# Kernel optimization log

Measured on AMD Instinct MI355X. Metric: run time of the kernel, lower is better.

Reference implementation:

```python
import jax, jax.numpy as jnp
import numpy as np

TEMP1 = 4.0  # local_temp1 default


def setup_inputs() -> dict:
    key = jax.random.key(0)
    k1, k2 = jax.random.split(key)
    query = jax.random.normal(k1, (256, 768, 96), dtype=jnp.float32)
    context = jax.random.normal(k2, (256, 768, 19, 19), dtype=jnp.float32)
    return {"query": query, "context": context}


def reference(query, context):
    # query: [B, ndf, Q]; context: [B, ndf, ih, iw]
    B, ndf, Q = query.shape
    ih, iw = context.shape[2], context.shape[3]
    S = ih * iw
    ctx = context.reshape(B, ndf, S)            # [B, ndf, S]
    # attn = contextT @ query -> [B, S, Q]
    attn = jnp.einsum('bds,bdq->bsq', ctx, query)
    # softmax over query dim
    attn = jax.nn.softmax(attn, axis=-1)
    # transpose to [B, Q, S], temperature scale, softmax over source dim
    attn = jnp.swapaxes(attn, 1, 2) * TEMP1
    attn = jax.nn.softmax(attn, axis=-1)        # [B, Q, S]
    # weightedContext = context @ attn^T -> [B, ndf, Q]
    weighted_context = jnp.einsum('bds,bqs->bdq', ctx, attn)
    attn_map = attn.reshape(B, Q, ih, iw)
    return weighted_context, attn_map
```

## Files before the change

### kernel.cpp

```cpp
#include <hip/hip_runtime.h>

#define NB 256
#define NDF 768
#define NQ 96
#define NS 361
#define LDT 40
#define LDP 392
#define WSROW 368
#define WS_BYTES ((size_t)NB * NQ * WSROW * 2)

typedef short bf16x8_t __attribute__((ext_vector_type(8)));
typedef float f32x4_t __attribute__((ext_vector_type(4)));
typedef float f32x4u_t __attribute__((ext_vector_type(4), aligned(4)));
typedef unsigned int u32x2_t __attribute__((ext_vector_type(2)));
typedef unsigned int u32x4_t __attribute__((ext_vector_type(4)));

__device__ __forceinline__ unsigned pack_hi(unsigned b_, unsigned a_) {
    return __builtin_amdgcn_perm(b_, a_, 0x07060302u);
}
__device__ __forceinline__ unsigned short f2bf(float x) {
    unsigned u = __float_as_uint(x);
    u += 0x7FFFu + ((u >> 16) & 1u);
    return (unsigned short)(u >> 16);
}
__device__ __forceinline__ float bf2f(unsigned short h) {
    return __uint_as_float(((unsigned)h) << 16);
}

template<bool WSP>
__global__ __launch_bounds__(384, 3) void k1_gemm1_softmaxq(
    const float* __restrict__ Qg, const float* __restrict__ Cg,
    unsigned short* __restrict__ Wsb, float* __restrict__ AoutF)
{
    __shared__ unsigned short sQhi[NQ * LDT];
    __shared__ unsigned short sQlo[NQ * LDT];
    __shared__ unsigned short sShi[192 * LDT];
    __shared__ unsigned short sSlo[192 * LDT];

    const int b = blockIdx.x >> 1;
    const int h = blockIdx.x & 1;
    const int tid = threadIdx.x;
    const int wv = tid >> 6;
    const int lane = tid & 63;
    const int ll = lane & 15;
    const int lg = lane >> 4;
    const int s0 = 192 * h;
    const int qq  = tid % NQ;
    const int kqQ = tid / NQ;
    const int ssb = tid % 192;
    const int kqC = tid / 192;
    const int sAbs = s0 + ssb;
    const bool okC = (sAbs < NS);

    const float* __restrict__ qg = Qg + (size_t)b * NDF * NQ;
    const float* __restrict__ cg = Cg + (size_t)b * NDF * NS;

    f32x4_t acc[6][2];
#pragma unroll
    for (int i = 0; i < 6; ++i)
#pragma unroll
        for (int j = 0; j < 2; ++j) acc[i][j] = (f32x4_t)0.0f;

    float RQa[8], RCa[16], RQb[8], RCb[16];

#define LOADQ(K0, R) { \
    const float* p = qg + ((K0) + 4 * kqQ) * NQ + qq; \
    R[0] = p[0]; R[1] = p[NQ]; R[2] = p[2 * NQ]; R[3] = p[3 * NQ]; \
    const float* p2 = p + 16 * NQ; \
    R[4] = p2[0]; R[5] = p2[NQ]; R[6] = p2[2 * NQ]; R[7] = p2[3 * NQ]; }

#define LOADC(K0, R) { \
    const float* p = cg + ((K0) + 4 * kqC) * NS + sAbs; \
    _Pragma("unroll") \
    for (int j = 0; j < 4; ++j) { \
        const float* pj = p + j * 8 * NS; \
        R[4*j+0] = okC ? pj[0] : 0.0f; \
        R[4*j+1] = okC ? pj[NS] : 0.0f; \
        R[4*j+2] = okC ? pj[2*NS] : 0.0f; \
        R[4*j+3] = okC ? pj[3*NS] : 0.0f; } }

#define STOREQC(RQ, RC) { \
    _Pragma("unroll") \
    for (int t = 0; t < 2; ++t) { \
        unsigned u0 = __float_as_uint(RQ[4*t+0]), u1 = __float_as_uint(RQ[4*t+1]); \
        unsigned u2 = __float_as_uint(RQ[4*t+2]), u3 = __float_as_uint(RQ[4*t+3]); \
        float l0 = RQ[4*t+0] - __uint_as_float(u0 & 0xFFFF0000u); \
        float l1 = RQ[4*t+1] - __uint_as_float(u1 & 0xFFFF0000u); \
        float l2 = RQ[4*t+2] - __uint_as_float(u2 & 0xFFFF0000u); \
        float l3 = RQ[4*t+3] - __uint_as_float(u3 & 0xFFFF0000u); \
        u32x2_t hi, lo; \
        hi[0] = pack_hi(u1, u0); hi[1] = pack_hi(u3, u2); \
        lo[0] = pack_hi(__float_as_uint(l1), __float_as_uint(l0)); \
        lo[1] = pack_hi(__float_as_uint(l3), __float_as_uint(l2)); \
        int off = qq * LDT + 4 * (kqQ + 4 * t); \
        *(u32x2_t*)&sQhi[off] = hi; \
        *(u32x2_t*)&sQlo[off] = lo; } \
    _Pragma("unroll") \
    for (int j = 0; j < 4; ++j) { \
        unsigned u0 = __float_as_uint(RC[4*j+0]), u1 = __float_as_uint(RC[4*j+1]); \
        unsigned u2 = __float_as_uint(RC[4*j+2]), u3 = __float_as_uint(RC[4*j+3]); \
        float l0 = RC[4*j+0] - __uint_as_float(u0 & 0xFFFF0000u); \
        float l1 = RC[4*j+1] - __uint_as_float(u1 & 0xFFFF0000u); \
        float l2 = RC[4*j+2] - __uint_as_float(u2 & 0xFFFF0000u); \
        float l3 = RC[4*j+3] - __uint_as_float(u3 & 0xFFFF0000u); \
        u32x2_t hi, lo; \
        hi[0] = pack_hi(u1, u0); hi[1] = pack_hi(u3, u2); \
        lo[0] = pack_hi(__float_as_uint(l1), __float_as_uint(l0)); \
        lo[1] = pack_hi(__float_as_uint(l3), __float_as_uint(l2)); \
        int off = ssb * LDT + 4 * (kqC + 2 * j); \
        *(u32x2_t*)&sShi[off] = hi; \
        *(u32x2_t*)&sSlo[off] = lo; } }

#define FRAGMFMA() { \
    bf16x8_t Bhi[2], Blo[2]; \
    _Pragma("unroll") \
    for (int nt = 0; nt < 2; ++nt) { \
        int row = 32 * wv + 16 * nt + ll; \
        Bhi[nt] = *(const bf16x8_t*)&sShi[row * LDT + 8 * lg]; \
        Blo[nt] = *(const bf16x8_t*)&sSlo[row * LDT + 8 * lg]; } \
    _Pragma("unroll") \
    for (int mt = 0; mt < 6; ++mt) { \
        int row = 16 * mt + ll; \
        bf16x8_t Ahi = *(const bf16x8_t*)&sQhi[row * LDT + 8 * lg]; \
        bf16x8_t Alo = *(const bf16x8_t*)&sQlo[row * LDT + 8 * lg]; \
        _Pragma("unroll") \
        for (int nt = 0; nt < 2; ++nt) { \
            acc[mt][nt] = __builtin_amdgcn_mfma_f32_16x16x32_bf16(Ahi, Bhi[nt], acc[mt][nt], 0, 0, 0); \
            acc[mt][nt] = __builtin_amdgcn_mfma_f32_16x16x32_bf16(Ahi, Blo[nt], acc[mt][nt], 0, 0, 0); \
            acc[mt][nt] = __builtin_amdgcn_mfma_f32_16x16x32_bf16(Alo, Bhi[nt], acc[mt][nt], 0, 0, 0); } } }

    LOADQ(0, RQa); LOADC(0, RCa);
    for (int k0 = 0; k0 < NDF; k0 += 64) {
        STOREQC(RQa, RCa);
        __syncthreads();
        if (k0 + 32 < NDF) { LOADQ(k0 + 32, RQb); LOADC(k0 + 32, RCb); }
        FRAGMFMA();
        __syncthreads();
        STOREQC(RQb, RCb);
        __syncthreads();
        if (k0 + 64 < NDF) { LOADQ(k0 + 64, RQa); LOADC(k0 + 64, RCa); }
        FRAGMFMA();
        __syncthreads();
    }
#undef LOADQ
#undef LOADC
#undef STOREQC
#undef FRAGMFMA

#pragma unroll
    for (int nt = 0; nt < 2; ++nt) {
        float m = -3.0e38f;
#pragma unroll
        for (int mt = 0; mt < 6; ++mt)
#pragma unroll
            for (int r = 0; r < 4; ++r) m = fmaxf(m, acc[mt][nt][r]);
        m = fmaxf(m, __shfl_xor(m, 16));
        m = fmaxf(m, __shfl_xor(m, 32));
        float sum = 0.0f;
#pragma unroll
        for (int mt = 0; mt < 6; ++mt)
#pragma unroll
            for (int r = 0; r < 4; ++r) {
                float e = __expf(acc[mt][nt][r] - m);
                acc[mt][nt][r] = e;
                sum += e;
            }
        sum += __shfl_xor(sum, 16);
        sum += __shfl_xor(sum, 32);
        float inv = 4.0f / sum;
#pragma unroll
        for (int mt = 0; mt < 6; ++mt)
#pragma unroll
            for (int r = 0; r < 4; ++r) acc[mt][nt][r] *= inv;
    }

    if constexpr (WSP) {
        unsigned short* wr = Wsb + (size_t)b * NQ * WSROW;
#pragma unroll
        for (int mt = 0; mt < 6; ++mt)
#pragma unroll
            for (int nt = 0; nt < 2; ++nt)
#pragma unroll
                for (int r = 0; r < 4; ++r) {
                    int q = 16 * mt + 4 * lg + r;
                    int s = s0 + 32 * wv + 16 * nt + ll;
                    if (s < NS) wr[q * WSROW + s] = f2bf(acc[mt][nt][r]);
                }
    } else {
        float* aout = AoutF + (size_t)b * NQ * NS;
#pragma unroll
        for (int mt = 0; mt < 6; ++mt)
#pragma unroll
            for (int nt = 0; nt < 2; ++nt)
#pragma unroll
                for (int r = 0; r < 4; ++r) {
                    int q = 16 * mt + 4 * lg + r;
                    int s = s0 + 32 * wv + 16 * nt + ll;
                    if (s < NS) aout[(size_t)q * NS + s] = acc[mt][nt][r];
                }
    }
}

__global__ __launch_bounds__(256) void k15_softmaxs(float* __restrict__ Aout)
{
    const int b = blockIdx.x;
    const int q = blockIdx.y * 4 + (threadIdx.x >> 6);
    const int lane = threadIdx.x & 63;
    float* __restrict__ row = Aout + ((size_t)b * NQ + q) * NS;
    const int c0 = 6 * lane;

    float v[6];
    if (c0 + 5 < NS) {
        f32x4u_t t = *(const f32x4u_t*)(row + c0);
        v[0] = t[0]; v[1] = t[1]; v[2] = t[2]; v[3] = t[3];
        v[4] = row[c0 + 4]; v[5] = row[c0 + 5];
    } else {
#pragma unroll
        for (int i = 0; i < 6; ++i) v[i] = (c0 + i < NS) ? row[c0 + i] : -INFINITY;
    }
    float m = v[0];
#pragma unroll
    for (int i = 1; i < 6; ++i) m = fmaxf(m, v[i]);
#pragma unroll
    for (int o = 1; o < 64; o <<= 1) m = fmaxf(m, __shfl_xor(m, o));
    float e[6], sum = 0.0f;
#pragma unroll
    for (int i = 0; i < 6; ++i) { e[i] = __expf(v[i] - m); sum += e[i]; }
#pragma unroll
    for (int o = 1; o < 64; o <<= 1) sum += __shfl_xor(sum, o);
    float inv = 1.0f / sum;
#pragma unroll
    for (int i = 0; i < 6; ++i) if (c0 + i < NS) row[c0 + i] = e[i] * inv;
}

template<bool FUSED>
__global__ __launch_bounds__(512, 4) void k2_gemm2(
    const float* __restrict__ Cg, const unsigned short* __restrict__ Wsb,
    const float* __restrict__ AttnF, float* __restrict__ Wout, float* __restrict__ AoutF)
{
    extern __shared__ char smem2[];
    unsigned short* sP = (unsigned short*)smem2;
    unsigned* sPd = (unsigned*)smem2;
    float* sMax = (float*)(smem2 + NQ * LDP * 2);
    float* sInv = sMax + NQ;

    const int b = blockIdx.x >> 2;
    const int quarter = blockIdx.x & 3;
    const int tid = threadIdx.x;
    const int wv = tid >> 6;
    const int lane = tid & 63;
    const int ll = lane & 15;
    const int lg = lane >> 4;

    if constexpr (FUSED) {
        const unsigned* __restrict__ wsd = (const unsigned*)(Wsb + (size_t)b * NQ * WSROW);
        for (int i = tid; i < NQ * 184; i += 512) {
            int r = i / 184, c = i - r * 184;
            sPd[r * 196 + c] = wsd[i];
        }
        for (int i = tid; i < NQ * 12; i += 512) {
            int r = i / 12, c = i - r * 12;
            sPd[r * 196 + 184 + c] = 0;
        }
        __syncthreads();

        const int l32 = tid & 31;
        const int rbase = tid >> 5;
#pragma unroll
        for (int pass = 0; pass < 6; ++pass) {
            int row = pass * 16 + rbase;
            float m = -3.0e38f;
#pragma unroll
            for (int j = 0; j < 6; ++j) {
                int dw = l32 + 32 * j;
                if (dw < 184) {
                    unsigned u = sPd[row * 196 + dw];
                    float v0 = bf2f((unsigned short)(u & 0xFFFFu));
                    float v1 = bf2f((unsigned short)(u >> 16));
                    if (2 * dw < NS) m = fmaxf(m, v0);
                    if (2 * dw + 1 < NS) m = fmaxf(m, v1);
                }
            }
#pragma unroll
            for (int o = 1; o < 32; o <<= 1) m = fmaxf(m, __shfl_xor(m, o));
            if (l32 == 0) sMax[row] = m;
        }
        __syncthreads();
#pragma unroll
        for (int pass = 0; pass < 6; ++pass) {
            int row = pass * 16 + rbase;
            float m = sMax[row];
            float sum = 0.0f;
#pragma unroll
            for (int j = 0; j < 6; ++j) {
                int dw = l32 + 32 * j;
                if (dw < 184) {
                    unsigned u = sPd[row * 196 + dw];
                    float v0 = bf2f((unsigned short)(u & 0xFFFFu));
                    float v1 = bf2f((unsigned short)(u >> 16));
                    float e0 = (2 * dw < NS) ? __expf(v0 - m) : 0.0f;
                    float e1 = (2 * dw + 1 < NS) ? __expf(v1 - m) : 0.0f;
                    sum += e0 + e1;
                    sPd[row * 196 + dw] = ((unsigned)f2bf(e1) << 16) | (unsigned)f2bf(e0);
                }
            }
#pragma unroll
            for (int o = 1; o < 32; o <<= 1) sum += __shfl_xor(sum, o);
            if (l32 == 0) sInv[row] = sum;
        }
        __syncthreads();
        if (tid < NQ) sInv[tid] = 1.0f / sInv[tid];
        __syncthreads();
        if (quarter == 0) {
            float* aout = AoutF + (size_t)b * NQ * NS;
            for (int i = tid; i < NQ * NS; i += 512) {
                int q = i / NS, s = i - q * NS;
                aout[i] = bf2f(sP[q * LDP + s]) * sInv[q];
            }
        }
    } else {
        const float* __restrict__ attn = AttnF + (size_t)b * NQ * NS;
        for (int i = tid; i < NQ * 181; i += 512) {
            int row = i / 181, p = i - row * 181;
            float x0 = attn[row * NS + 2 * p];
            float x1 = (p < 180) ? attn[row * NS + 2 * p + 1] : 0.0f;
            unsigned r0 = __float_as_uint(x0) + 0x8000u;
            unsigned r1 = __float_as_uint(x1) + 0x8000u;
            sPd[row * 196 + p] = pack_hi(r1, r0);
        }
        for (int i = tid; i < NQ * 15; i += 512) {
            int row = i / 15, p = i - row * 15;
            sPd[row * 196 + 181 + p] = 0;
        }
        __syncthreads();
    }

    f32x4_t acc[3][3];
#pragma unroll
    for (int i = 0; i < 3; ++i)
#pragma unroll
        for (int j = 0; j < 3; ++j) acc[i][j] = (f32x4_t)0.0f;

    const float* __restrict__ cq = Cg + (size_t)b * NDF * NS + (size_t)(quarter * 192) * NS;
    const int dw = wv >> 1, qw = wv & 1;

#pragma unroll
    for (int c = 0; c < 12; ++c) {
        bf16x8_t Bf[3];
#pragma unroll
        for (int nt = 0; nt < 3; ++nt) {
            int row = 16 * (3 * qw + nt) + ll;
            Bf[nt] = *(const bf16x8_t*)&sP[row * LDP + 32 * c + 8 * lg];
        }
#pragma unroll
        for (int i = 0; i < 3; ++i) {
            int d = 16 * (3 * dw + i) + ll;
            const float* ap = cq + (size_t)d * NS + 32 * c + 8 * lg;
            u32x4_t u;
            if (c < 11) {
                f32x4u_t a0 = *(const f32x4u_t*)ap;
                f32x4u_t a1 = *(const f32x4u_t*)(ap + 4);
                u[0] = pack_hi(__float_as_uint(a0[1]), __float_as_uint(a0[0]));
                u[1] = pack_hi(__float_as_uint(a0[3]), __float_as_uint(a0[2]));
                u[2] = pack_hi(__float_as_uint(a1[1]), __float_as_uint(a1[0]));
                u[3] = pack_hi(__float_as_uint(a1[3]), __float_as_uint(a1[2]));
            } else {
                float t[8];
#pragma unroll
                for (int e = 0; e < 8; ++e) {
                    int s = 352 + 8 * lg + e;
                    t[e] = (s < NS) ? ap[e] : 0.0f;
                }
                u[0] = pack_hi(__float_as_uint(t[1]), __float_as_uint(t[0]));
                u[1] = pack_hi(__float_as_uint(t[3]), __float_as_uint(t[2]));
                u[2] = pack_hi(__float_as_uint(t[5]), __float_as_uint(t[4]));
                u[3] = pack_hi(__float_as_uint(t[7]), __float_as_uint(t[6]));
            }
            bf16x8_t Af = __builtin_bit_cast(bf16x8_t, u);
#pragma unroll
            for (int nt = 0; nt < 3; ++nt)
                acc[i][nt] = __builtin_amdgcn_mfma_f32_16x16x32_bf16(Af, Bf[nt], acc[i][nt], 0, 0, 0);
        }
    }

    float* wout = Wout + (size_t)b * NDF * NQ;
    float invq[3];
#pragma unroll
    for (int nt = 0; nt < 3; ++nt) {
        if constexpr (FUSED) invq[nt] = sInv[16 * (3 * qw + nt) + ll];
        else invq[nt] = 1.0f;
    }
#pragma unroll
    for (int i = 0; i < 3; ++i)
#pragma unroll
        for (int nt = 0; nt < 3; ++nt)
#pragma unroll
            for (int r = 0; r < 4; ++r) {
                int d = quarter * 192 + 16 * (3 * dw + i) + 4 * lg + r;
                int q = 16 * (3 * qw + nt) + ll;
                wout[(size_t)d * NQ + q] = acc[i][nt][r] * invq[nt];
            }
}

extern "C" void kernel_launch(void* const* d_in, const int* in_sizes, int n_in,
                              void* d_out, int out_size, void* d_ws, size_t ws_size,
                              hipStream_t stream) {
    const float* Qg = (const float*)d_in[0];
    const float* Cg = (const float*)d_in[1];
    float* Wout = (float*)d_out;
    float* Aout = Wout + (size_t)NB * NDF * NQ;

    const int smem2 = NQ * LDP * 2 + NQ * 8;

    if (ws_size >= WS_BYTES) {
        unsigned short* wsb = (unsigned short*)d_ws;
        k1_gemm1_softmaxq<true><<<dim3(NB * 2), dim3(384), 0, stream>>>(Qg, Cg, wsb, nullptr);
        (void)hipFuncSetAttribute((const void*)k2_gemm2<true>,
                                  hipFuncAttributeMaxDynamicSharedMemorySize, smem2);
        k2_gemm2<true><<<dim3(NB * 4), dim3(512), smem2, stream>>>(Cg, wsb, nullptr, Wout, Aout);
    } else {
        k1_gemm1_softmaxq<false><<<dim3(NB * 2), dim3(384), 0, stream>>>(Qg, Cg, nullptr, Aout);
        k15_softmaxs<<<dim3(NB, 24), dim3(256), 0, stream>>>(Aout);
        (void)hipFuncSetAttribute((const void*)k2_gemm2<false>,
                                  hipFuncAttributeMaxDynamicSharedMemorySize, smem2);
        k2_gemm2<false><<<dim3(NB * 4), dim3(512), smem2, stream>>>(Cg, nullptr, Aout, Wout, Aout);
    }
}
```

Measured before the change: 229.4 us.

## Cache bf16 context in workspace from k1 so k2 reads half the bytes

Kernel 1, which already reads the fp32 context for the first GEMM, now also writes a truncated bf16 copy of it into a padded workspace buffer. Kernel 2 then loads bf16 fragments directly instead of re-reading and packing the fp32 context. This halves the context read traffic in k2 but adds a write of the same size in k1. The C-load mapping also changes so each thread handles two adjacent source columns, and the fallback paths change their rounding and load code slightly. This path only runs when the workspace is large enough to hold the copy.

```diff
diff --git a/kernel.cpp b/kernel.cpp
--- a/kernel.cpp
+++ b/kernel.cpp
@@ -7,7 +7,10 @@
 #define LDT 40
 #define LDP 392
 #define WSROW 368
-#define WS_BYTES ((size_t)NB * NQ * WSROW * 2)
+#define CSROW 368
+#define WS_LOG_BYTES ((size_t)NB * NQ * WSROW * 2)
+#define WS_CTX_BYTES ((size_t)NB * NDF * CSROW * 2)
+#define WS_FULL_BYTES (WS_LOG_BYTES + WS_CTX_BYTES)
 
 typedef short bf16x8_t __attribute__((ext_vector_type(8)));
 typedef float f32x4_t __attribute__((ext_vector_type(4)));
@@ -27,10 +30,11 @@
     return __uint_as_float(((unsigned)h) << 16);
 }
 
-template<bool WSP>
+template<int MODE>
 __global__ __launch_bounds__(384, 3) void k1_gemm1_softmaxq(
     const float* __restrict__ Qg, const float* __restrict__ Cg,
-    unsigned short* __restrict__ Wsb, float* __restrict__ AoutF)
+    unsigned short* __restrict__ WsLog, unsigned* __restrict__ WsCtxD,
+    float* __restrict__ AoutF)
 {
     __shared__ unsigned short sQhi[NQ * LDT];
     __shared__ unsigned short sQlo[NQ * LDT];
@@ -47,13 +51,17 @@
     const int s0 = 192 * h;
     const int qq  = tid % NQ;
     const int kqQ = tid / NQ;
-    const int ssb = tid % 192;
-    const int kqC = tid / 192;
-    const int sAbs = s0 + ssb;
-    const bool okC = (sAbs < NS);
+    const int sp  = tid % 96;
+    const int kqb = tid / 96;
+    const int sA0 = s0 + 2 * sp;
+    const bool ok0 = (sA0 < NS);
+    const bool ok1 = (sA0 + 1 < NS);
+    const int wsCol = 96 * h + sp;
+    const bool wok = (MODE == 2) && (wsCol < 184);
 
     const float* __restrict__ qg = Qg + (size_t)b * NDF * NQ;
     const float* __restrict__ cg = Cg + (size_t)b * NDF * NS;
+    unsigned* __restrict__ wscd = (MODE == 2) ? (WsCtxD + (size_t)b * NDF * 184) : nullptr;
 
     f32x4_t acc[6][2];
 #pragma unroll
@@ -61,7 +69,8 @@
 #pragma unroll
         for (int j = 0; j < 2; ++j) acc[i][j] = (f32x4_t)0.0f;
 
-    float RQa[8], RCa[16], RQb[8], RCb[16];
+    float RQa[8], RQb[8];
+    float RCa[16], RCb[16];
 
 #define LOADQ(K0, R) { \
     const float* p = qg + ((K0) + 4 * kqQ) * NQ + qq; \
@@ -70,46 +79,58 @@
     R[4] = p2[0]; R[5] = p2[NQ]; R[6] = p2[2 * NQ]; R[7] = p2[3 * NQ]; }
 
 #define LOADC(K0, R) { \
-    const float* p = cg + ((K0) + 4 * kqC) * NS + sAbs; \
     _Pragma("unroll") \
-    for (int j = 0; j < 4; ++j) { \
-        const float* pj = p + j * 8 * NS; \
-        R[4*j+0] = okC ? pj[0] : 0.0f; \
-        R[4*j+1] = okC ? pj[NS] : 0.0f; \
-        R[4*j+2] = okC ? pj[2*NS] : 0.0f; \
-        R[4*j+3] = okC ? pj[3*NS] : 0.0f; } }
-
-#define STOREQC(RQ, RC) { \
+    for (int k2 = 0; k2 < 2; ++k2) { \
+        const float* p = cg + ((K0) + 4 * (kqb + 4 * k2)) * NS; \
+        _Pragma("unroll") \
+        for (int j = 0; j < 4; ++j) { \
+            const float* pj = p + j * NS; \
+            R[(k2 * 4 + j) * 2 + 0] = ok0 ? pj[sA0] : 0.0f; \
+            R[(k2 * 4 + j) * 2 + 1] = ok1 ? pj[sA0 + 1] : 0.0f; } } }
+
+#define STOREQ(R) { \
     _Pragma("unroll") \
     for (int t = 0; t < 2; ++t) { \
-        unsigned u0 = __float_as_uint(RQ[4*t+0]), u1 = __float_as_uint(RQ[4*t+1]); \
-        unsigned u2 = __float_as_uint(RQ[4*t+2]), u3 = __float_as_uint(RQ[4*t+3]); \
-        float l0 = RQ[4*t+0] - __uint_as_float(u0 & 0xFFFF0000u); \
-        float l1 = RQ[4*t+1] - __uint_as_float(u1 & 0xFFFF0000u); \
-        float l2 = RQ[4*t+2] - __uint_as_float(u2 & 0xFFFF0000u); \
-        float l3 = RQ[4*t+3] - __uint_as_float(u3 & 0xFFFF0000u); \
+        unsigned u0 = __float_as_uint(R[4*t+0]), u1 = __float_as_uint(R[4*t+1]); \
+        unsigned u2 = __float_as_uint(R[4*t+2]), u3 = __float_as_uint(R[4*t+3]); \
+        float l0 = R[4*t+0] - __uint_as_float(u0 & 0xFFFF0000u); \
+        float l1 = R[4*t+1] - __uint_as_float(u1 & 0xFFFF0000u); \
+        float l2 = R[4*t+2] - __uint_as_float(u2 & 0xFFFF0000u); \
+        float l3 = R[4*t+3] - __uint_as_float(u3 & 0xFFFF0000u); \
         u32x2_t hi, lo; \
         hi[0] = pack_hi(u1, u0); hi[1] = pack_hi(u3, u2); \
         lo[0] = pack_hi(__float_as_uint(l1), __float_as_uint(l0)); \
         lo[1] = pack_hi(__float_as_uint(l3), __float_as_uint(l2)); \
         int off = qq * LDT + 4 * (kqQ + 4 * t); \
         *(u32x2_t*)&sQhi[off] = hi; \
-        *(u32x2_t*)&sQlo[off] = lo; } \
+        *(u32x2_t*)&sQlo[off] = lo; } }
+
+#define STOREC(K0, R) { \
     _Pragma("unroll") \
-    for (int j = 0; j < 4; ++j) { \
-        unsigned u0 = __float_as_uint(RC[4*j+0]), u1 = __float_as_uint(RC[4*j+1]); \
-        unsigned u2 = __float_as_uint(RC[4*j+2]), u3 = __float_as_uint(RC[4*j+3]); \
-        float l0 = RC[4*j+0] - __uint_as_float(u0 & 0xFFFF0000u); \
-        float l1 = RC[4*j+1] - __uint_as_float(u1 & 0xFFFF0000u); \
-        float l2 = RC[4*j+2] - __uint_as_float(u2 & 0xFFFF0000u); \
-        float l3 = RC[4*j+3] - __uint_as_float(u3 & 0xFFFF0000u); \
-        u32x2_t hi, lo; \
-        hi[0] = pack_hi(u1, u0); hi[1] = pack_hi(u3, u2); \
-        lo[0] = pack_hi(__float_as_uint(l1), __float_as_uint(l0)); \
-        lo[1] = pack_hi(__float_as_uint(l3), __float_as_uint(l2)); \
-        int off = ssb * LDT + 4 * (kqC + 2 * j); \
-        *(u32x2_t*)&sShi[off] = hi; \
-        *(u32x2_t*)&sSlo[off] = lo; } }
+    for (int k2 = 0; k2 < 2; ++k2) { \
+        const int kq = kqb + 4 * k2; \
+        unsigned u[4][2]; float l[4][2]; \
+        _Pragma("unroll") \
+        for (int j = 0; j < 4; ++j) { \
+            _Pragma("unroll") \
+            for (int s1 = 0; s1 < 2; ++s1) { \
+                float x = R[(k2 * 4 + j) * 2 + s1]; \
+                u[j][s1] = __float_as_uint(x); \
+                l[j][s1] = x - __uint_as_float(u[j][s1] & 0xFFFF0000u); } } \
+        _Pragma("unroll") \
+        for (int s1 = 0; s1 < 2; ++s1) { \
+            u32x2_t hi, lo; \
+            hi[0] = pack_hi(u[1][s1], u[0][s1]); \
+            hi[1] = pack_hi(u[3][s1], u[2][s1]); \
+            lo[0] = pack_hi(__float_as_uint(l[1][s1]), __float_as_uint(l[0][s1])); \
+            lo[1] = pack_hi(__float_as_uint(l[3][s1]), __float_as_uint(l[2][s1])); \
+            int off = (2 * sp + s1) * LDT + 4 * kq; \
+            *(u32x2_t*)&sShi[off] = hi; \
+            *(u32x2_t*)&sSlo[off] = lo; } \
+        if (wok) { \
+            _Pragma("unroll") \
+            for (int j = 0; j < 4; ++j) \
+                wscd[(size_t)((K0) + 4 * kq + j) * 184 + wsCol] = pack_hi(u[j][1], u[j][0]); } } }
 
 #define FRAGMFMA() { \
     bf16x8_t Bhi[2], Blo[2]; \
@@ -131,12 +152,12 @@
 
     LOADQ(0, RQa); LOADC(0, RCa);
     for (int k0 = 0; k0 < NDF; k0 += 64) {
-        STOREQC(RQa, RCa);
+        STOREQ(RQa); STOREC(k0, RCa);
         __syncthreads();
         if (k0 + 32 < NDF) { LOADQ(k0 + 32, RQb); LOADC(k0 + 32, RCb); }
         FRAGMFMA();
         __syncthreads();
-        STOREQC(RQb, RCb);
+        STOREQ(RQb); STOREC(k0 + 32, RCb);
         __syncthreads();
         if (k0 + 64 < NDF) { LOADQ(k0 + 64, RQa); LOADC(k0 + 64, RCa); }
         FRAGMFMA();
@@ -144,7 +165,8 @@
     }
 #undef LOADQ
 #undef LOADC
-#undef STOREQC
+#undef STOREQ
+#undef STOREC
 #undef FRAGMFMA
 
 #pragma unroll
@@ -174,8 +196,8 @@
             for (int r = 0; r < 4; ++r) acc[mt][nt][r] *= inv;
     }
 
-    if constexpr (WSP) {
-        unsigned short* wr = Wsb + (size_t)b * NQ * WSROW;
+    if constexpr (MODE >= 1) {
+        unsigned short* wr = WsLog + (size_t)b * NQ * WSROW;
 #pragma unroll
         for (int mt = 0; mt < 6; ++mt)
 #pragma unroll
@@ -210,14 +232,8 @@
     const int c0 = 6 * lane;
 
     float v[6];
-    if (c0 + 5 < NS) {
-        f32x4u_t t = *(const f32x4u_t*)(row + c0);
-        v[0] = t[0]; v[1] = t[1]; v[2] = t[2]; v[3] = t[3];
-        v[4] = row[c0 + 4]; v[5] = row[c0 + 5];
-    } else {
-#pragma unroll
-        for (int i = 0; i < 6; ++i) v[i] = (c0 + i < NS) ? row[c0 + i] : -INFINITY;
-    }
+#pragma unroll
+    for (int i = 0; i < 6; ++i) v[i] = (c0 + i < NS) ? row[c0 + i] : -INFINITY;
     float m = v[0];
 #pragma unroll
     for (int i = 1; i < 6; ++i) m = fmaxf(m, v[i]);
@@ -233,9 +249,10 @@
     for (int i = 0; i < 6; ++i) if (c0 + i < NS) row[c0 + i] = e[i] * inv;
 }
 
-template<bool FUSED>
+template<int MODE>
 __global__ __launch_bounds__(512, 4) void k2_gemm2(
-    const float* __restrict__ Cg, const unsigned short* __restrict__ Wsb,
+    const float* __restrict__ Cg, const unsigned short* __restrict__ WsLog,
+    const unsigned short* __restrict__ WsCtx,
     const float* __restrict__ AttnF, float* __restrict__ Wout, float* __restrict__ AoutF)
 {
     extern __shared__ char smem2[];
@@ -252,8 +269,8 @@
     const int ll = lane & 15;
     const int lg = lane >> 4;
 
-    if constexpr (FUSED) {
-        const unsigned* __restrict__ wsd = (const unsigned*)(Wsb + (size_t)b * NQ * WSROW);
+    if constexpr (MODE >= 1) {
+        const unsigned* __restrict__ wsd = (const unsigned*)(WsLog + (size_t)b * NQ * WSROW);
         for (int i = tid; i < NQ * 184; i += 512) {
             int r = i / 184, c = i - r * 184;
             sPd[r * 196 + c] = wsd[i];
@@ -324,9 +341,7 @@
             int row = i / 181, p = i - row * 181;
             float x0 = attn[row * NS + 2 * p];
             float x1 = (p < 180) ? attn[row * NS + 2 * p + 1] : 0.0f;
-            unsigned r0 = __float_as_uint(x0) + 0x8000u;
-            unsigned r1 = __float_as_uint(x1) + 0x8000u;
-            sPd[row * 196 + p] = pack_hi(r1, r0);
+            sPd[row * 196 + p] = pack_hi(__float_as_uint(x1), __float_as_uint(x0));
         }
         for (int i = tid; i < NQ * 15; i += 512) {
             int row = i / 15, p = i - row * 15;
@@ -341,8 +356,10 @@
 #pragma unroll
         for (int j = 0; j < 3; ++j) acc[i][j] = (f32x4_t)0.0f;
 
+    const int dw = wv >> 1, qw = wv & 1;
     const float* __restrict__ cq = Cg + (size_t)b * NDF * NS + (size_t)(quarter * 192) * NS;
-    const int dw = wv >> 1, qw = wv & 1;
+    const unsigned short* __restrict__ cb =
+        (MODE == 2) ? (WsCtx + ((size_t)b * NDF + quarter * 192) * CSROW) : nullptr;
 
 #pragma unroll
     for (int c = 0; c < 12; ++c) {
@@ -355,28 +372,37 @@
 #pragma unroll
         for (int i = 0; i < 3; ++i) {
             int d = 16 * (3 * dw + i) + ll;
-            const float* ap = cq + (size_t)d * NS + 32 * c + 8 * lg;
-            u32x4_t u;
-            if (c < 11) {
-                f32x4u_t a0 = *(const f32x4u_t*)ap;
-                f32x4u_t a1 = *(const f32x4u_t*)(ap + 4);
-                u[0] = pack_hi(__float_as_uint(a0[1]), __float_as_uint(a0[0]));
-                u[1] = pack_hi(__float_as_uint(a0[3]), __float_as_uint(a0[2]));
-                u[2] = pack_hi(__float_as_uint(a1[1]), __float_as_uint(a1[0]));
-                u[3] = pack_hi(__float_as_uint(a1[3]), __float_as_uint(a1[2]));
+            bf16x8_t Af;
+            if constexpr (MODE == 2) {
+                if (c < 11 || lg < 2) {
+                    Af = *(const bf16x8_t*)&cb[(size_t)d * CSROW + 32 * c + 8 * lg];
+                } else {
+                    Af = (bf16x8_t)0;
+                }
             } else {
-                float t[8];
-#pragma unroll
-                for (int e = 0; e < 8; ++e) {
-                    int s = 352 + 8 * lg + e;
-                    t[e] = (s < NS) ? ap[e] : 0.0f;
-                }
-                u[0] = pack_hi(__float_as_uint(t[1]), __float_as_uint(t[0]));
-                u[1] = pack_hi(__float_as_uint(t[3]), __float_as_uint(t[2]));
-                u[2] = pack_hi(__float_as_uint(t[5]), __float_as_uint(t[4]));
-                u[3] = pack_hi(__float_as_uint(t[7]), __float_as_uint(t[6]));
-            }
-            bf16x8_t Af = __builtin_bit_cast(bf16x8_t, u);
+                const float* ap = cq + (size_t)d * NS + 32 * c + 8 * lg;
+                u32x4_t u;
+                if (c < 11) {
+                    f32x4u_t a0 = *(const f32x4u_t*)ap;
+                    f32x4u_t a1 = *(const f32x4u_t*)(ap + 4);
+                    u[0] = pack_hi(__float_as_uint(a0[1]), __float_as_uint(a0[0]));
+                    u[1] = pack_hi(__float_as_uint(a0[3]), __float_as_uint(a0[2]));
+                    u[2] = pack_hi(__float_as_uint(a1[1]), __float_as_uint(a1[0]));
+                    u[3] = pack_hi(__float_as_uint(a1[3]), __float_as_uint(a1[2]));
+                } else {
+                    float t[8];
+#pragma unroll
+                    for (int e = 0; e < 8; ++e) {
+                        int s = 352 + 8 * lg + e;
+                        t[e] = (s < NS) ? ap[e] : 0.0f;
+                    }
+                    u[0] = pack_hi(__float_as_uint(t[1]), __float_as_uint(t[0]));
+                    u[1] = pack_hi(__float_as_uint(t[3]), __float_as_uint(t[2]));
+                    u[2] = pack_hi(__float_as_uint(t[5]), __float_as_uint(t[4]));
+                    u[3] = pack_hi(__float_as_uint(t[7]), __float_as_uint(t[6]));
+                }
+                Af = __builtin_bit_cast(bf16x8_t, u);
+            }
 #pragma unroll
             for (int nt = 0; nt < 3; ++nt)
                 acc[i][nt] = __builtin_amdgcn_mfma_f32_16x16x32_bf16(Af, Bf[nt], acc[i][nt], 0, 0, 0);
@@ -387,7 +413,7 @@
     float invq[3];
 #pragma unroll
     for (int nt = 0; nt < 3; ++nt) {
-        if constexpr (FUSED) invq[nt] = sInv[16 * (3 * qw + nt) + ll];
+        if constexpr (MODE >= 1) invq[nt] = sInv[16 * (3 * qw + nt) + ll];
         else invq[nt] = 1.0f;
     }
 #pragma unroll
@@ -412,17 +438,27 @@
 
     const int smem2 = NQ * LDP * 2 + NQ * 8;
 
-    if (ws_size >= WS_BYTES) {
-        unsigned short* wsb = (unsigned short*)d_ws;
-        k1_gemm1_softmaxq<true><<<dim3(NB * 2), dim3(384), 0, stream>>>(Qg, Cg, wsb, nullptr);
-        (void)hipFuncSetAttribute((const void*)k2_gemm2<true>,
+    if (ws_size >= WS_FULL_BYTES) {
+        unsigned short* wsLog = (unsigned short*)d_ws;
+        unsigned* wsCtxD = (unsigned*)((char*)d_ws + WS_LOG_BYTES);
+        k1_gemm1_softmaxq<2><<<dim3(NB * 2), dim3(384), 0, stream>>>(Qg, Cg, wsLog, wsCtxD, nullptr);
+        (void)hipFuncSetAttribute((const void*)k2_gemm2<2>,
                                   hipFuncAttributeMaxDynamicSharedMemorySize, smem2);
-        k2_gemm2<true><<<dim3(NB * 4), dim3(512), smem2, stream>>>(Cg, wsb, nullptr, Wout, Aout);
+        k2_gemm2<2><<<dim3(NB * 4), dim3(512), smem2, stream>>>(
+            Cg, wsLog, (const unsigned short*)wsCtxD, nullptr, Wout, Aout);
+    } else if (ws_size >= WS_LOG_BYTES) {
+        unsigned short* wsLog = (unsigned short*)d_ws;
+        k1_gemm1_softmaxq<1><<<dim3(NB * 2), dim3(384), 0, stream>>>(Qg, Cg, wsLog, nullptr, nullptr);
+        (void)hipFuncSetAttribute((const void*)k2_gemm2<1>,
+                                  hipFuncAttributeMaxDynamicSharedMemorySize, smem2);
+        k2_gemm2<1><<<dim3(NB * 4), dim3(512), smem2, stream>>>(
+            Cg, wsLog, nullptr, nullptr, Wout, Aout);
     } else {
-        k1_gemm1_softmaxq<false><<<dim3(NB * 2), dim3(384), 0, stream>>>(Qg, Cg, nullptr, Aout);
+        k1_gemm1_softmaxq<0><<<dim3(NB * 2), dim3(384), 0, stream>>>(Qg, Cg, nullptr, nullptr, Aout);
         k15_softmaxs<<<dim3(NB, 24), dim3(256), 0, stream>>>(Aout);
-        (void)hipFuncSetAttribute((const void*)k2_gemm2<false>,
+        (void)hipFuncSetAttribute((const void*)k2_gemm2<0>,
                                   hipFuncAttributeMaxDynamicSharedMemorySize, smem2);
-        k2_gemm2<false><<<dim3(NB * 4), dim3(512), smem2, stream>>>(Cg, nullptr, Aout, Wout, Aout);
-    }
-}
+        k2_gemm2<0><<<dim3(NB * 4), dim3(512), smem2, stream>>>(
+            Cg, nullptr, nullptr, Aout, Wout, Aout);
+    }
+}
```

Result: no change. 233.4 us (+1.8%).

## Load context fragments directly into registers and double-buffer only query in LDS

Applied to the files above, without the earlier changes.

The first GEMM kernel stops staging the context tile through shared memory. Each wave now reads its own context columns from global memory straight into MFMA B-fragments, while only the query tile is split into hi/lo bf16 and double-buffered in LDS. This cuts one barrier per k-step and reduces LDS traffic and footprint. Block indices in both kernels are also remapped so that consecutive blocks spread across batches, probably to balance across XCDs and caches. The trade-off is strided, uncoalesced global reads of the context (8 rows per lane). The fallback path also changes its rounding to truncation.

```diff
diff --git a/kernel.cpp b/kernel.cpp
--- a/kernel.cpp
+++ b/kernel.cpp
@@ -7,12 +7,11 @@
 #define LDT 40
 #define LDP 392
 #define WSROW 368
-#define WS_BYTES ((size_t)NB * NQ * WSROW * 2)
+#define WS_LOG_BYTES ((size_t)NB * NQ * WSROW * 2)
 
 typedef short bf16x8_t __attribute__((ext_vector_type(8)));
 typedef float f32x4_t __attribute__((ext_vector_type(4)));
 typedef float f32x4u_t __attribute__((ext_vector_type(4), aligned(4)));
-typedef unsigned int u32x2_t __attribute__((ext_vector_type(2)));
 typedef unsigned int u32x4_t __attribute__((ext_vector_type(4)));
 
 __device__ __forceinline__ unsigned pack_hi(unsigned b_, unsigned a_) {
@@ -27,30 +26,55 @@
     return __uint_as_float(((unsigned)h) << 16);
 }
 
-template<bool WSP>
+__device__ __forceinline__ void cvt8(const float* x, bf16x8_t& hi, bf16x8_t& lo) {
+    unsigned uh[8]; float fl[8];
+#pragma unroll
+    for (int j = 0; j < 8; ++j) {
+        unsigned u = __float_as_uint(x[j]);
+        uh[j] = u;
+        fl[j] = x[j] - __uint_as_float(u & 0xFFFF0000u);
+    }
+    u32x4_t h, l;
+    h[0] = pack_hi(uh[1], uh[0]); h[1] = pack_hi(uh[3], uh[2]);
+    h[2] = pack_hi(uh[5], uh[4]); h[3] = pack_hi(uh[7], uh[6]);
+    l[0] = pack_hi(__float_as_uint(fl[1]), __float_as_uint(fl[0]));
+    l[1] = pack_hi(__float_as_uint(fl[3]), __float_as_uint(fl[2]));
+    l[2] = pack_hi(__float_as_uint(fl[5]), __float_as_uint(fl[4]));
+    l[3] = pack_hi(__float_as_uint(fl[7]), __float_as_uint(fl[6]));
+    hi = __builtin_bit_cast(bf16x8_t, h);
+    lo = __builtin_bit_cast(bf16x8_t, l);
+}
+
+__device__ __forceinline__ void block_sync_lds() {
+    __builtin_amdgcn_sched_barrier(0x20);
+    asm volatile("s_waitcnt lgkmcnt(0)" ::: "memory");
+    __builtin_amdgcn_sched_barrier(0x20);
+    __builtin_amdgcn_s_barrier();
+    __builtin_amdgcn_sched_barrier(0x20);
+}
+
+template<int MODE>
 __global__ __launch_bounds__(384, 3) void k1_gemm1_softmaxq(
     const float* __restrict__ Qg, const float* __restrict__ Cg,
-    unsigned short* __restrict__ Wsb, float* __restrict__ AoutF)
+    unsigned short* __restrict__ WsLog, float* __restrict__ AoutF)
 {
-    __shared__ unsigned short sQhi[NQ * LDT];
-    __shared__ unsigned short sQlo[NQ * LDT];
-    __shared__ unsigned short sShi[192 * LDT];
-    __shared__ unsigned short sSlo[192 * LDT];
-
-    const int b = blockIdx.x >> 1;
-    const int h = blockIdx.x & 1;
+    __shared__ __align__(16) unsigned short sQhi[2][NQ * LDT];
+    __shared__ __align__(16) unsigned short sQlo[2][NQ * LDT];
+
+    const int x = blockIdx.x;
+    const int b = (x & 7) * 32 + (x >> 4);
+    const int h = (x >> 3) & 1;
+
     const int tid = threadIdx.x;
     const int wv = tid >> 6;
     const int lane = tid & 63;
     const int ll = lane & 15;
     const int lg = lane >> 4;
     const int s0 = 192 * h;
-    const int qq  = tid % NQ;
-    const int kqQ = tid / NQ;
-    const int ssb = tid % 192;
-    const int kqC = tid / 192;
-    const int sAbs = s0 + ssb;
-    const bool okC = (sAbs < NS);
+    const int qq = tid % 96;
+    const int koct = tid / 96;
+    const int sc0 = min(s0 + 32 * wv + ll, NS - 1);
+    const int sc1 = min(s0 + 32 * wv + 16 + ll, NS - 1);
 
     const float* __restrict__ qg = Qg + (size_t)b * NDF * NQ;
     const float* __restrict__ cg = Cg + (size_t)b * NDF * NS;
@@ -61,91 +85,50 @@
 #pragma unroll
         for (int j = 0; j < 2; ++j) acc[i][j] = (f32x4_t)0.0f;
 
-    float RQa[8], RCa[16], RQb[8], RCb[16];
-
-#define LOADQ(K0, R) { \
-    const float* p = qg + ((K0) + 4 * kqQ) * NQ + qq; \
-    R[0] = p[0]; R[1] = p[NQ]; R[2] = p[2 * NQ]; R[3] = p[3 * NQ]; \
-    const float* p2 = p + 16 * NQ; \
-    R[4] = p2[0]; R[5] = p2[NQ]; R[6] = p2[2 * NQ]; R[7] = p2[3 * NQ]; }
-
-#define LOADC(K0, R) { \
-    const float* p = cg + ((K0) + 4 * kqC) * NS + sAbs; \
+    float rq[8];
+
+#define LOADQ(K0) { \
     _Pragma("unroll") \
-    for (int j = 0; j < 4; ++j) { \
-        const float* pj = p + j * 8 * NS; \
-        R[4*j+0] = okC ? pj[0] : 0.0f; \
-        R[4*j+1] = okC ? pj[NS] : 0.0f; \
-        R[4*j+2] = okC ? pj[2*NS] : 0.0f; \
-        R[4*j+3] = okC ? pj[3*NS] : 0.0f; } }
-
-#define STOREQC(RQ, RC) { \
-    _Pragma("unroll") \
-    for (int t = 0; t < 2; ++t) { \
-        unsigned u0 = __float_as_uint(RQ[4*t+0]), u1 = __float_as_uint(RQ[4*t+1]); \
-        unsigned u2 = __float_as_uint(RQ[4*t+2]), u3 = __float_as_uint(RQ[4*t+3]); \
-        float l0 = RQ[4*t+0] - __uint_as_float(u0 & 0xFFFF0000u); \
-        float l1 = RQ[4*t+1] - __uint_as_float(u1 & 0xFFFF0000u); \
-        float l2 = RQ[4*t+2] - __uint_as_float(u2 & 0xFFFF0000u); \
-        float l3 = RQ[4*t+3] - __uint_as_float(u3 & 0xFFFF0000u); \
-        u32x2_t hi, lo; \
-        hi[0] = pack_hi(u1, u0); hi[1] = pack_hi(u3, u2); \
-        lo[0] = pack_hi(__float_as_uint(l1), __float_as_uint(l0)); \
-        lo[1] = pack_hi(__float_as_uint(l3), __float_as_uint(l2)); \
-        int off = qq * LDT + 4 * (kqQ + 4 * t); \
-        *(u32x2_t*)&sQhi[off] = hi; \
-        *(u32x2_t*)&sQlo[off] = lo; } \
-    _Pragma("unroll") \
-    for (int j = 0; j < 4; ++j) { \
-        unsigned u0 = __float_as_uint(RC[4*j+0]), u1 = __float_as_uint(RC[4*j+1]); \
-        unsigned u2 = __float_as_uint(RC[4*j+2]), u3 = __float_as_uint(RC[4*j+3]); \
-        float l0 = RC[4*j+0] - __uint_as_float(u0 & 0xFFFF0000u); \
-        float l1 = RC[4*j+1] - __uint_as_float(u1 & 0xFFFF0000u); \
-        float l2 = RC[4*j+2] - __uint_as_float(u2 & 0xFFFF0000u); \
-        float l3 = RC[4*j+3] - __uint_as_float(u3 & 0xFFFF0000u); \
-        u32x2_t hi, lo; \
-        hi[0] = pack_hi(u1, u0); hi[1] = pack_hi(u3, u2); \
-        lo[0] = pack_hi(__float_as_uint(l1), __float_as_uint(l0)); \
-        lo[1] = pack_hi(__float_as_uint(l3), __float_as_uint(l2)); \
-        int off = ssb * LDT + 4 * (kqC + 2 * j); \
-        *(u32x2_t*)&sShi[off] = hi; \
-        *(u32x2_t*)&sSlo[off] = lo; } }
-
-#define FRAGMFMA() { \
-    bf16x8_t Bhi[2], Blo[2]; \
-    _Pragma("unroll") \
-    for (int nt = 0; nt < 2; ++nt) { \
-        int row = 32 * wv + 16 * nt + ll; \
-        Bhi[nt] = *(const bf16x8_t*)&sShi[row * LDT + 8 * lg]; \
-        Blo[nt] = *(const bf16x8_t*)&sSlo[row * LDT + 8 * lg]; } \
-    _Pragma("unroll") \
-    for (int mt = 0; mt < 6; ++mt) { \
-        int row = 16 * mt + ll; \
-        bf16x8_t Ahi = *(const bf16x8_t*)&sQhi[row * LDT + 8 * lg]; \
-        bf16x8_t Alo = *(const bf16x8_t*)&sQlo[row * LDT + 8 * lg]; \
-        _Pragma("unroll") \
-        for (int nt = 0; nt < 2; ++nt) { \
-            acc[mt][nt] = __builtin_amdgcn_mfma_f32_16x16x32_bf16(Ahi, Bhi[nt], acc[mt][nt], 0, 0, 0); \
-            acc[mt][nt] = __builtin_amdgcn_mfma_f32_16x16x32_bf16(Ahi, Blo[nt], acc[mt][nt], 0, 0, 0); \
-            acc[mt][nt] = __builtin_amdgcn_mfma_f32_16x16x32_bf16(Alo, Bhi[nt], acc[mt][nt], 0, 0, 0); } } }
-
-    LOADQ(0, RQa); LOADC(0, RCa);
-    for (int k0 = 0; k0 < NDF; k0 += 64) {
-        STOREQC(RQa, RCa);
-        __syncthreads();
-        if (k0 + 32 < NDF) { LOADQ(k0 + 32, RQb); LOADC(k0 + 32, RCb); }
-        FRAGMFMA();
-        __syncthreads();
-        STOREQC(RQb, RCb);
-        __syncthreads();
-        if (k0 + 64 < NDF) { LOADQ(k0 + 64, RQa); LOADC(k0 + 64, RCa); }
-        FRAGMFMA();
-        __syncthreads();
+    for (int j = 0; j < 8; ++j) \
+        rq[j] = qg[((K0) + 8 * koct + j) * NQ + qq]; }
+
+#define STAGEQ(BUF) { \
+    bf16x8_t qh, ql; \
+    cvt8(rq, qh, ql); \
+    *(bf16x8_t*)&sQhi[BUF][qq * LDT + 8 * koct] = qh; \
+    *(bf16x8_t*)&sQlo[BUF][qq * LDT + 8 * koct] = ql; }
+
+    LOADQ(0);
+    STAGEQ(0);
+    block_sync_lds();
+
+    for (int k0 = 0; k0 < NDF; k0 += 32) {
+        const int cur = (k0 >> 5) & 1;
+        float c0v[8], c1v[8];
+#pragma unroll
+        for (int j = 0; j < 8; ++j) c0v[j] = cg[(size_t)(k0 + 8 * lg + j) * NS + sc0];
+#pragma unroll
+        for (int j = 0; j < 8; ++j) c1v[j] = cg[(size_t)(k0 + 8 * lg + j) * NS + sc1];
+        if (k0 + 32 < NDF) LOADQ(k0 + 32);
+        bf16x8_t B0h, B0l, B1h, B1l;
+        cvt8(c0v, B0h, B0l);
+        cvt8(c1v, B1h, B1l);
+#pragma unroll
+        for (int mt = 0; mt < 6; ++mt) {
+            bf16x8_t Ah = *(const bf16x8_t*)&sQhi[cur][(16 * mt + ll) * LDT + 8 * lg];
+            bf16x8_t Al = *(const bf16x8_t*)&sQlo[cur][(16 * mt + ll) * LDT + 8 * lg];
+            acc[mt][0] = __builtin_amdgcn_mfma_f32_16x16x32_bf16(Ah, B0h, acc[mt][0], 0, 0, 0);
+            acc[mt][0] = __builtin_amdgcn_mfma_f32_16x16x32_bf16(Ah, B0l, acc[mt][0], 0, 0, 0);
+            acc[mt][0] = __builtin_amdgcn_mfma_f32_16x16x32_bf16(Al, B0h, acc[mt][0], 0, 0, 0);
+            acc[mt][1] = __builtin_amdgcn_mfma_f32_16x16x32_bf16(Ah, B1h, acc[mt][1], 0, 0, 0);
+            acc[mt][1] = __builtin_amdgcn_mfma_f32_16x16x32_bf16(Ah, B1l, acc[mt][1], 0, 0, 0);
+            acc[mt][1] = __builtin_amdgcn_mfma_f32_16x16x32_bf16(Al, B1h, acc[mt][1], 0, 0, 0);
+        }
+        if (k0 + 32 < NDF) STAGEQ(cur ^ 1);
+        block_sync_lds();
     }
 #undef LOADQ
-#undef LOADC
-#undef STOREQC
-#undef FRAGMFMA
+#undef STAGEQ
 
 #pragma unroll
     for (int nt = 0; nt < 2; ++nt) {
@@ -174,8 +157,8 @@
             for (int r = 0; r < 4; ++r) acc[mt][nt][r] *= inv;
     }
 
-    if constexpr (WSP) {
-        unsigned short* wr = Wsb + (size_t)b * NQ * WSROW;
+    if constexpr (MODE >= 1) {
+        unsigned short* wr = WsLog + (size_t)b * NQ * WSROW;
 #pragma unroll
         for (int mt = 0; mt < 6; ++mt)
 #pragma unroll
@@ -210,14 +193,8 @@
     const int c0 = 6 * lane;
 
     float v[6];
-    if (c0 + 5 < NS) {
-        f32x4u_t t = *(const f32x4u_t*)(row + c0);
-        v[0] = t[0]; v[1] = t[1]; v[2] = t[2]; v[3] = t[3];
-        v[4] = row[c0 + 4]; v[5] = row[c0 + 5];
-    } else {
-#pragma unroll
-        for (int i = 0; i < 6; ++i) v[i] = (c0 + i < NS) ? row[c0 + i] : -INFINITY;
-    }
+#pragma unroll
+    for (int i = 0; i < 6; ++i) v[i] = (c0 + i < NS) ? row[c0 + i] : -INFINITY;
     float m = v[0];
 #pragma unroll
     for (int i = 1; i < 6; ++i) m = fmaxf(m, v[i]);
@@ -235,7 +212,7 @@
 
 template<bool FUSED>
 __global__ __launch_bounds__(512, 4) void k2_gemm2(
-    const float* __restrict__ Cg, const unsigned short* __restrict__ Wsb,
+    const float* __restrict__ Cg, const unsigned short* __restrict__ WsLog,
     const float* __restrict__ AttnF, float* __restrict__ Wout, float* __restrict__ AoutF)
 {
     extern __shared__ char smem2[];
@@ -244,8 +221,9 @@
     float* sMax = (float*)(smem2 + NQ * LDP * 2);
     float* sInv = sMax + NQ;
 
-    const int b = blockIdx.x >> 2;
-    const int quarter = blockIdx.x & 3;
+    const int x = blockIdx.x;
+    const int b = (x & 7) * 32 + (x >> 5);
+    const int quarter = (x >> 3) & 3;
     const int tid = threadIdx.x;
     const int wv = tid >> 6;
     const int lane = tid & 63;
@@ -253,7 +231,7 @@
     const int lg = lane >> 4;
 
     if constexpr (FUSED) {
-        const unsigned* __restrict__ wsd = (const unsigned*)(Wsb + (size_t)b * NQ * WSROW);
+        const unsigned* __restrict__ wsd = (const unsigned*)(WsLog + (size_t)b * NQ * WSROW);
         for (int i = tid; i < NQ * 184; i += 512) {
             int r = i / 184, c = i - r * 184;
             sPd[r * 196 + c] = wsd[i];
@@ -324,9 +302,7 @@
             int row = i / 181, p = i - row * 181;
             float x0 = attn[row * NS + 2 * p];
             float x1 = (p < 180) ? attn[row * NS + 2 * p + 1] : 0.0f;
-            unsigned r0 = __float_as_uint(x0) + 0x8000u;
-            unsigned r1 = __float_as_uint(x1) + 0x8000u;
-            sPd[row * 196 + p] = pack_hi(r1, r0);
+            sPd[row * 196 + p] = pack_hi(__float_as_uint(x1), __float_as_uint(x0));
         }
         for (int i = tid; i < NQ * 15; i += 512) {
             int row = i / 15, p = i - row * 15;
@@ -341,8 +317,8 @@
 #pragma unroll
         for (int j = 0; j < 3; ++j) acc[i][j] = (f32x4_t)0.0f;
 
+    const int dw = wv >> 1, qw = wv & 1;
     const float* __restrict__ cq = Cg + (size_t)b * NDF * NS + (size_t)(quarter * 192) * NS;
-    const int dw = wv >> 1, qw = wv & 1;
 
 #pragma unroll
     for (int c = 0; c < 12; ++c) {
@@ -412,17 +388,19 @@
 
     const int smem2 = NQ * LDP * 2 + NQ * 8;
 
-    if (ws_size >= WS_BYTES) {
-        unsigned short* wsb = (unsigned short*)d_ws;
-        k1_gemm1_softmaxq<true><<<dim3(NB * 2), dim3(384), 0, stream>>>(Qg, Cg, wsb, nullptr);
+    if (ws_size >= WS_LOG_BYTES) {
+        unsigned short* wsLog = (unsigned short*)d_ws;
+        k1_gemm1_softmaxq<1><<<dim3(NB * 2), dim3(384), 0, stream>>>(Qg, Cg, wsLog, nullptr);
         (void)hipFuncSetAttribute((const void*)k2_gemm2<true>,
                                   hipFuncAttributeMaxDynamicSharedMemorySize, smem2);
-        k2_gemm2<true><<<dim3(NB * 4), dim3(512), smem2, stream>>>(Cg, wsb, nullptr, Wout, Aout);
+        k2_gemm2<true><<<dim3(NB * 4), dim3(512), smem2, stream>>>(
+            Cg, wsLog, nullptr, Wout, Aout);
     } else {
-        k1_gemm1_softmaxq<false><<<dim3(NB * 2), dim3(384), 0, stream>>>(Qg, Cg, nullptr, Aout);
+        k1_gemm1_softmaxq<0><<<dim3(NB * 2), dim3(384), 0, stream>>>(Qg, Cg, nullptr, Aout);
         k15_softmaxs<<<dim3(NB, 24), dim3(256), 0, stream>>>(Aout);
         (void)hipFuncSetAttribute((const void*)k2_gemm2<false>,
                                   hipFuncAttributeMaxDynamicSharedMemorySize, smem2);
-        k2_gemm2<false><<<dim3(NB * 4), dim3(512), smem2, stream>>>(Cg, nullptr, Aout, Wout, Aout);
-    }
-}
+        k2_gemm2<false><<<dim3(NB * 4), dim3(512), smem2, stream>>>(
+            Cg, nullptr, Aout, Wout, Aout);
+    }
+}
```

Measured after the change: 209.0 us. 1.1x faster.
